# Kernel optimization log

Measured on AMD Instinct MI355X. Metric: run time of the kernel, lower is better.

The kernel has to match this reference:

```python
import jax, jax.numpy as jnp
import numpy as np

B, S, H, D = 16, 512, 12, 64          # batch, seq, heads, head_dim
HID = H * D                            # 768
MAX_POS = 512
CHAR_HP = 0.5
WORD_HP = 0.5


def setup_inputs() -> dict:
    key = jax.random.key(0)
    ks = jax.random.split(key, 12)
    s = 0.02
    return {
        "hidden_states": jax.random.normal(ks[0], (B, S, HID), jnp.float32),
        "attention_mask": jnp.zeros((B, 1, 1, S), jnp.float32),
        "character_level_matrix": jax.random.randint(ks[1], (B, S, S), 0, 8),
        "word_level_matrix": jax.random.randint(ks[2], (B, S, S), 0, 8),
        "Wq": jax.random.normal(ks[3], (HID, HID), jnp.float32) * s,
        "bq": jnp.zeros((HID,), jnp.float32),
        "Wk": jax.random.normal(ks[4], (HID, HID), jnp.float32) * s,
        "bk": jnp.zeros((HID,), jnp.float32),
        "Wv": jax.random.normal(ks[5], (HID, HID), jnp.float32) * s,
        "bv": jnp.zeros((HID,), jnp.float32),
        "dist_emb": jax.random.normal(ks[6], (2 * MAX_POS - 1, D), jnp.float32) * s,
        "char_emb": jax.random.normal(ks[7], (8, 1), jnp.float32) * s,
        "word_emb": jax.random.normal(ks[8], (8, 1), jnp.float32) * s,
    }


def reference(hidden_states, attention_mask, character_level_matrix,
              word_level_matrix, Wq, bq, Wk, bk, Wv, bv,
              dist_emb, char_emb, word_emb):
    # level nn-embedding lookup: [B,S,S] int -> [B,S,S] float
    char_bias = char_emb[character_level_matrix][..., 0]
    word_bias = word_emb[word_level_matrix][..., 0]

    def heads(x):  # [B,S,HID] -> [B,H,S,D]
        return x.reshape(B, S, H, D).transpose(0, 2, 1, 3)

    q = heads(hidden_states @ Wq.T + bq)
    k = heads(hidden_states @ Wk.T + bk)
    v = heads(hidden_states @ Wv.T + bv)

    scores = jnp.einsum('bhld,bhrd->bhlr', q, k)
    # level biases broadcast over heads
    scores = scores + CHAR_HP * char_bias[:, None] + WORD_HP * word_bias[:, None]

    # relative_key_query positional scores
    pos = jnp.arange(S)
    distance = pos[:, None] - pos[None, :]
    pe = dist_emb[distance + MAX_POS - 1]  # [S(l), S(r), D]
    scores = scores + jnp.einsum('bhld,lrd->bhlr', q, pe) \
                    + jnp.einsum('bhrd,lrd->bhlr', k, pe)

    scores = scores / jnp.sqrt(jnp.float32(D)) + attention_mask
    probs = jax.nn.softmax(scores, axis=-1)
    ctx = jnp.einsum('bhlr,bhrd->bhld', probs, v)
    return ctx.transpose(0, 2, 1, 3).reshape(B, S, HID)
```

## Files before the change

kernel.cpp:

```cpp
#include <hip/hip_runtime.h>
#include <stdint.h>

#define Bv 16
#define Sv 512
#define Hv 12
#define Dv 64
#define HIDv 768

typedef __attribute__((ext_vector_type(8))) short bf8_t;
typedef __attribute__((ext_vector_type(4))) float f32x4;
typedef __attribute__((ext_vector_type(8))) unsigned short u16x8;
typedef __attribute__((ext_vector_type(4))) unsigned short u16x4;

__device__ __forceinline__ float b2f(unsigned short u){
    union { unsigned int i; float f; } x; x.i = ((unsigned int)u) << 16; return x.f;
}
__device__ __forceinline__ unsigned short f2b(float f){
    union { float f; unsigned int i; } x; x.f = f;
    unsigned int r = x.i + 0x7fff + ((x.i >> 16) & 1);
    return (unsigned short)(r >> 16);
}
__device__ __forceinline__ void gload16(const unsigned short* g, unsigned short* l){
    __builtin_amdgcn_global_load_lds(
        (const __attribute__((address_space(1))) void*)g,
        (__attribute__((address_space(3))) void*)l, 16, 0, 0);
}

#define RS 0.18033688f
#define LOG2E 1.44269504f

__global__ void cvt_bf16(const float* __restrict__ src, unsigned short* __restrict__ dst, int n4){
    int i = blockIdx.x * 256 + threadIdx.x;
    int stride = gridDim.x * 256;
    for (; i < n4; i += stride){
        float4 v = ((const float4*)src)[i];
        u16x4 o = { f2b(v.x), f2b(v.y), f2b(v.z), f2b(v.w) };
        ((u16x4*)dst)[i] = o;
    }
}

__global__ void cvt_w3(const float* __restrict__ a, const float* __restrict__ b,
                       const float* __restrict__ c, unsigned short* __restrict__ dst, int n4each){
    int i = blockIdx.x * 256 + threadIdx.x;
    if (i >= 3*n4each) return;
    int which = i / n4each, j = i - which*n4each;
    const float* src = which == 0 ? a : (which == 1 ? b : c);
    float4 v = ((const float4*)src)[j];
    u16x4 o = { f2b(v.x), f2b(v.y), f2b(v.z), f2b(v.w) };
    ((u16x4*)dst)[i] = o;
}

__global__ __launch_bounds__(256) void prep_bias_t(
    const int* __restrict__ cmat, const int* __restrict__ wmat,
    const float* __restrict__ mask, const float* __restrict__ ce, const float* __restrict__ we,
    unsigned short* __restrict__ lvlt)
{
    __shared__ float tab[64];
    const int t = threadIdx.x;
    const int blk = blockIdx.x;
    const int c8 = blk & 7, lt = (blk >> 3) & 7, b = blk >> 6;
    if (t < 64) tab[t] = (0.5f*ce[t>>3] + 0.5f*we[t&7]) * RS;
    __syncthreads();
    const int w = t >> 6, lane = t & 63, g = lane >> 4, cc = lane & 15;
    const int ll = lt*64 + w*16 + cc;
    const int* crow = cmat + ((size_t)b*512 + ll)*512;
    const int* wrow = wmat + ((size_t)b*512 + ll)*512;
    const float* mrow = mask + (size_t)b*512;
    unsigned short o[16];
    #pragma unroll
    for (int i = 0; i < 4; ++i){
        int rb = c8*64 + i*16 + 4*g;
        int4 c4 = *(const int4*)(crow + rb);
        int4 w4 = *(const int4*)(wrow + rb);
        float4 mv = *(const float4*)(mrow + rb);
        o[i*4 + 0] = f2b(tab[(c4.x<<3)|w4.x] + mv.x * LOG2E);
        o[i*4 + 1] = f2b(tab[(c4.y<<3)|w4.y] + mv.y * LOG2E);
        o[i*4 + 2] = f2b(tab[(c4.z<<3)|w4.z] + mv.z * LOG2E);
        o[i*4 + 3] = f2b(tab[(c4.w<<3)|w4.w] + mv.w * LOG2E);
    }
    unsigned short* dst = lvlt + ((size_t)blk*256 + t)*16;
    *(u16x8*)dst       = *(u16x8*)&o[0];
    *(u16x8*)(dst + 8) = *(u16x8*)&o[8];
}

__global__ __launch_bounds__(256,3) void qkv_gemm(
    const unsigned short* __restrict__ Xb,
    const unsigned short* __restrict__ Wb,
    const float* __restrict__ bq, const float* __restrict__ bk, const float* __restrict__ bv,
    unsigned short* __restrict__ qkb,
    unsigned short* __restrict__ vtb)
{
    __shared__ unsigned short Ab[128*40];
    __shared__ unsigned short Bb[128*40];
    const int t = threadIdx.x;
    const int w = t >> 6, lane = t & 63, g = lane >> 4, cc = lane & 15;
    const int wm = w >> 1, wn = w & 1;
    const int m0 = blockIdx.x * 128;
    const int n0 = blockIdx.y * 128;

    const f32x4 fz = {0.f,0.f,0.f,0.f};
    f32x4 acc[4][4];
    #pragma unroll
    for (int i = 0; i < 4; ++i)
        #pragma unroll
        for (int j = 0; j < 4; ++j) acc[i][j] = fz;

    u16x8 pa[2], pb[2];
    #pragma unroll
    for (int r = 0; r < 2; ++r){
        int chunk = t + r*256; int row = chunk >> 2; int ch = chunk & 3;
        pa[r] = *(const u16x8*)(Xb + (size_t)(m0+row)*768 + ch*8);
        pb[r] = *(const u16x8*)(Wb + (size_t)(n0+row)*768 + ch*8);
    }
    for (int k0 = 0; k0 < 768; k0 += 32){
        __syncthreads();
        #pragma unroll
        for (int r = 0; r < 2; ++r){
            int chunk = t + r*256; int row = chunk >> 2; int ch = chunk & 3;
            *(u16x8*)&Ab[row*40 + ch*8] = pa[r];
            *(u16x8*)&Bb[row*40 + ch*8] = pb[r];
        }
        __syncthreads();
        if (k0 + 32 < 768){
            #pragma unroll
            for (int r = 0; r < 2; ++r){
                int chunk = t + r*256; int row = chunk >> 2; int ch = chunk & 3;
                pa[r] = *(const u16x8*)(Xb + (size_t)(m0+row)*768 + (k0+32) + ch*8);
                pb[r] = *(const u16x8*)(Wb + (size_t)(n0+row)*768 + (k0+32) + ch*8);
            }
        }
        bf8_t af[4], bfr[4];
        #pragma unroll
        for (int mf = 0; mf < 4; ++mf)
            af[mf] = *(const bf8_t*)&Ab[(wm*64 + mf*16 + cc)*40 + g*8];
        #pragma unroll
        for (int nf = 0; nf < 4; ++nf)
            bfr[nf] = *(const bf8_t*)&Bb[(wn*64 + nf*16 + cc)*40 + g*8];
        #pragma unroll
        for (int mf = 0; mf < 4; ++mf)
            #pragma unroll
            for (int nf = 0; nf < 4; ++nf)
                acc[mf][nf] = __builtin_amdgcn_mfma_f32_16x16x32_bf16(af[mf], bfr[nf], acc[mf][nf], 0,0,0);
    }

    const int b  = m0 >> 9;
    const int s0 = (m0 & 511) + wm*64;
    const int nbase = n0 + wn*64;
    const int proj = nbase / 768;
    const int nin0 = nbase % 768;
    const float* bias = proj == 0 ? bq : (proj == 1 ? bk : bv);
    #pragma unroll
    for (int nf = 0; nf < 4; ++nf){
        int nin = nin0 + nf*16 + cc;
        int h = nin >> 6, d = nin & 63;
        float bvv = bias[nin];
        #pragma unroll
        for (int mf = 0; mf < 4; ++mf){
            int s = s0 + mf*16 + g*4;
            if (proj < 2){
                unsigned short* base = qkb + (((((size_t)proj*Bv + b)*Hv + h)*Sv + s)*Dv + d);
                #pragma unroll
                for (int r2 = 0; r2 < 4; ++r2)
                    base[(size_t)r2*Dv] = f2b(acc[mf][nf][r2] + bvv);
            } else {
                u16x4 o = { f2b(acc[mf][nf][0]+bvv), f2b(acc[mf][nf][1]+bvv),
                            f2b(acc[mf][nf][2]+bvv), f2b(acc[mf][nf][3]+bvv) };
                *(u16x4*)(vtb + ((((size_t)b*Hv + h)*Dv + d)*Sv + s)) = o;
            }
        }
    }
}

__global__ __launch_bounds__(256,2) void attn(
    const unsigned short* __restrict__ qkb,
    const unsigned short* __restrict__ vtb,
    const unsigned short* __restrict__ deb,
    const unsigned short* __restrict__ lvlt,
    float* __restrict__ out)
{
    __shared__ __align__(16) unsigned short sm[37904];
    unsigned short* ks  = sm;
    unsigned short* vsq = sm + 4096;
    unsigned short* des = sm + 8192;
    float*          t1c = (float*)(sm + 16384);
    float*          t2c = (float*)(sm + 25360);
    unsigned int*   Pb  = (unsigned int*)(sm + 33808);

    const int t = threadIdx.x, w = t >> 6, lane = t & 63, g = lane >> 4, cc = lane & 15;
    const int lr8 = lane >> 3, lc8 = lane & 7;

    const int wg = blockIdx.x;
    const int xcd = wg & 7, inner = wg >> 3;
    const int b  = ((inner & 1) << 3) | xcd;
    const int r2 = inner >> 1;
    const int h  = r2 % 12, lt = r2 / 12;
    const int l0 = lt * 64;

    const unsigned short* qp = qkb + ((((size_t)0*Bv + b)*Hv + h)*Sv + l0)*Dv;
    const unsigned short* kp = qkb + ((((size_t)1*Bv + b)*Hv + h)*Sv)*Dv;
    const unsigned short* vp = vtb + (((size_t)b*Hv + h)*Dv)*Sv;
    const unsigned short* lvbase = lvlt + (((size_t)b*8 + lt)*8)*256*16 + (size_t)t*16;

    const f32x4 fz = {0.f,0.f,0.f,0.f};
    const int R   = 3 - w;
    const int llm = w*16 + cc;
    const int sw  = (cc & 7) << 2;
    const int d_t1 = cc - 4*g;
    const int s_t2 = 4*g + cc;

    auto stage_k = [&](int r0){
        #pragma unroll
        for (int j = 0; j < 2; ++j){
            int row = w*16 + j*8 + lr8;
            int ch  = lc8 ^ (row & 7);
            gload16(kp + (size_t)(r0 + row)*64 + ch*8, ks + w*1024 + j*512);
        }
    };
    auto stage_de = [&](int r0){
        const int base = l0 - r0 + 448;
        #pragma unroll
        for (int j = 0; j < 4; ++j){
            int row = w*32 + j*8 + lr8;
            int gr = base + row; if (gr > 1022) gr = 1022;
            int ch  = lc8 ^ (row & 7);
            gload16(deb + (size_t)gr*64 + ch*8, des + w*2048 + j*512);
        }
    };
    auto stage_v0 = [&](){
        #pragma unroll
        for (int j = 0; j < 2; ++j){
            int row = w*16 + j*8 + lr8;
            int ch  = lc8 ^ (row & 7);
            gload16(vp + (size_t)row*512 + ch*8, vsq + w*1024 + j*512);
        }
    };

    bf8_t qf0, qf1;
    {
        int qrow = w*16 + cc;
        qf0 = *(const bf8_t*)(qp + (size_t)qrow*64 + g*8);
        qf1 = *(const bf8_t*)(qp + (size_t)qrow*64 + (g+4)*8);
    }
    stage_k(0); stage_de(0); stage_v0();
    __syncthreads();

    float l_run = 0.f;
    f32x4 ctx[4] = {fz,fz,fz,fz};

    for (int c8 = 0; c8 < 8; ++c8){
        const int r0 = c8 * 64;
        u16x8 lva = *(const u16x8*)(lvbase + (size_t)c8*256*16);
        u16x8 lvb = *(const u16x8*)(lvbase + (size_t)c8*256*16 + 8);

        __builtin_amdgcn_s_setprio(1);
        f32x4 accs[4];
        bf8_t kf0, kf1;
        #pragma unroll
        for (int i = 0; i < 4; ++i){
            int row = i*16 + cc;
            bf8_t b0 = *(const bf8_t*)&ks[row*64 + ((g       ^ (row & 7))*8)];
            bf8_t b1 = *(const bf8_t*)&ks[row*64 + (((g + 4) ^ (row & 7))*8)];
            if (i == R){ kf0 = b0; kf1 = b1; }
            f32x4 a = fz;
            a = __builtin_amdgcn_mfma_f32_16x16x32_bf16(b0, qf0, a, 0,0,0);
            a = __builtin_amdgcn_mfma_f32_16x16x32_bf16(b1, qf1, a, 0,0,0);
            accs[i] = a;
        }
        #pragma unroll
        for (int i = 0; i < 5; ++i){
            int jrow = (w + i)*16 + cc;
            bf8_t d0 = *(const bf8_t*)&des[jrow*64 + ((g       ^ (jrow & 7))*8)];
            bf8_t d1 = *(const bf8_t*)&des[jrow*64 + (((g + 4) ^ (jrow & 7))*8)];
            f32x4 a1 = fz, a2 = fz;
            a1 = __builtin_amdgcn_mfma_f32_16x16x32_bf16(d0, qf0, a1, 0,0,0);
            a1 = __builtin_amdgcn_mfma_f32_16x16x32_bf16(d1, qf1, a1, 0,0,0);
            a2 = __builtin_amdgcn_mfma_f32_16x16x32_bf16(kf0, d0, a2, 0,0,0);
            a2 = __builtin_amdgcn_mfma_f32_16x16x32_bf16(kf1, d1, a2, 0,0,0);

            {
                float* tb = t1c + (cc - 16*i - 4*g + 61)*68 + llm;
                bool mA = (i != 0 || d_t1 <= 3) && (i != 4 || d_t1 >= 3);
                bool mB = (i != 0 || d_t1 <= 1) && (i != 4 || d_t1 >= 1);
                if (mA){ tb[0]   = a1[3]; tb[68]  = a1[2]; }
                if (mB){ tb[136] = a1[1]; tb[204] = a1[0]; }
            }
            {
                float* tb = t2c + (R*16 + 4*g)*66 + (16*i + 4*g + cc - 14);
                bool mA = (i != 0 || s_t2 >= 14) && (i != 4 || s_t2 <= 14);
                bool mB = (i != 0 || s_t2 >= 12) && (i != 4 || s_t2 <= 12);
                if (mA){ tb[0]   = a2[0]; tb[67]  = a2[1]; }
                if (mB){ tb[134] = a2[2]; tb[201] = a2[3]; }
            }
        }
        __builtin_amdgcn_s_setprio(0);
        __syncthreads();

        u16x8 pv0, pv1;
        if (c8 < 7){
            stage_k(r0 + 64); stage_de(r0 + 64);
            int row0 = w*16 + lr8,  ch0 = lc8 ^ (row0 & 7);
            int row1 = row0 + 8,    ch1 = lc8 ^ (row1 & 7);
            pv0 = *(const u16x8*)(vp + (size_t)row0*512 + (r0+64) + ch0*8);
            pv1 = *(const u16x8*)(vp + (size_t)row1*512 + (r0+64) + ch1*8);
        }

        float ps = 0.f;
        #pragma unroll
        for (int i = 0; i < 4; ++i){
            const float* g1 = t1c + (i*16 + 4*g + 1)*68 + llm;
            const float* g2 = t2c + (i*16 + 4*g)*66 + llm + 1;
            float t10 = g1[0], t11 = g1[68], t12 = g1[136], t13 = g1[204];
            float t20 = g2[0], t21 = g2[66], t22 = g2[132], t23 = g2[198];
            float lv0 = b2f(i < 2 ? (unsigned short)lva[i*4+0] : (unsigned short)lvb[(i-2)*4+0]);
            float lv1 = b2f(i < 2 ? (unsigned short)lva[i*4+1] : (unsigned short)lvb[(i-2)*4+1]);
            float lv2 = b2f(i < 2 ? (unsigned short)lva[i*4+2] : (unsigned short)lvb[(i-2)*4+2]);
            float lv3 = b2f(i < 2 ? (unsigned short)lva[i*4+3] : (unsigned short)lvb[(i-2)*4+3]);
            float p0 = __builtin_amdgcn_exp2f((accs[i][0] + t10 + t20) * RS + lv0);
            float p1 = __builtin_amdgcn_exp2f((accs[i][1] + t11 + t21) * RS + lv1);
            float p2 = __builtin_amdgcn_exp2f((accs[i][2] + t12 + t22) * RS + lv2);
            float p3 = __builtin_amdgcn_exp2f((accs[i][3] + t13 + t23) * RS + lv3);
            ps += (p0 + p1) + (p2 + p3);
            unsigned int prs0 = (unsigned)f2b(p0) | ((unsigned)f2b(p1) << 16);
            unsigned int prs1 = (unsigned)f2b(p2) | ((unsigned)f2b(p3) << 16);
            uint2 pr = { prs0, prs1 };
            *(uint2*)&Pb[llm*32 + ((i*8 + 2*g) ^ sw)] = pr;
        }
        ps += __shfl_xor(ps, 16);
        ps += __shfl_xor(ps, 32);
        l_run += ps;
        __builtin_amdgcn_wave_barrier();

        __builtin_amdgcn_s_setprio(1);
        #pragma unroll
        for (int kh = 0; kh < 2; ++kh){
            bf8_t pf = *(const bf8_t*)&Pb[llm*32 + ((16*kh + 4*g) ^ sw)];
            #pragma unroll
            for (int nf = 0; nf < 4; ++nf){
                int vr = nf*16 + cc;
                bf8_t vf = *(const bf8_t*)&vsq[vr*64 + (((g + 4*kh) ^ (vr & 7))*8)];
                ctx[nf] = __builtin_amdgcn_mfma_f32_16x16x32_bf16(pf, vf, ctx[nf], 0,0,0);
            }
        }
        __builtin_amdgcn_s_setprio(0);

        if (c8 < 7){
            __syncthreads();
            *(u16x8*)&vsq[w*1024 +       lane*8] = pv0;
            *(u16x8*)&vsq[w*1024 + 512 + lane*8] = pv1;
            __syncthreads();
        }
    }

    float linv[4];
    #pragma unroll
    for (int reg = 0; reg < 4; ++reg)
        linv[reg] = 1.0f / __shfl(l_run, 4*g + reg);

    #pragma unroll
    for (int nf = 0; nf < 4; ++nf){
        #pragma unroll
        for (int reg = 0; reg < 4; ++reg){
            int ll = w*16 + 4*g + reg;
            out[((size_t)b*Sv + l0 + ll)*HIDv + h*64 + nf*16 + cc] = ctx[nf][reg] * linv[reg];
        }
    }
}

extern "C" void kernel_launch(void* const* d_in, const int* in_sizes, int n_in,
                              void* d_out, int out_size, void* d_ws, size_t ws_size,
                              hipStream_t stream)
{
    const float* hs   = (const float*)d_in[0];
    const float* mask = (const float*)d_in[1];
    const int*   cmat = (const int*)  d_in[2];
    const int*   wmat = (const int*)  d_in[3];
    const float* Wq   = (const float*)d_in[4];
    const float* bq   = (const float*)d_in[5];
    const float* Wk   = (const float*)d_in[6];
    const float* bk   = (const float*)d_in[7];
    const float* Wv   = (const float*)d_in[8];
    const float* bv   = (const float*)d_in[9];
    const float* de   = (const float*)d_in[10];
    const float* ce   = (const float*)d_in[11];
    const float* we   = (const float*)d_in[12];
    float* out = (float*)d_out;

    unsigned short* Xb   = (unsigned short*)d_ws;
    unsigned short* Wb   = Xb   + 6291456;
    unsigned short* deb  = Wb   + 1769472;
    unsigned short* qkb  = deb  + 65536;
    unsigned short* vtb  = qkb  + 12582912;
    unsigned short* lvlt = vtb  + 6291456;

    cvt_bf16<<<2048, 256, 0, stream>>>(hs, Xb, 1572864);
    cvt_w3<<<1728, 256, 0, stream>>>(Wq, Wk, Wv, Wb, 147456);
    cvt_bf16<<<64,   256, 0, stream>>>(de, deb, 16368);
    prep_bias_t<<<1024, 256, 0, stream>>>(cmat, wmat, mask, ce, we, lvlt);

    qkv_gemm<<<dim3(64, 18), 256, 0, stream>>>(Xb, Wb, bq, bk, bv, qkb, vtb);
    attn<<<1536, 256, 0, stream>>>(qkb, vtb, deb, lvlt, out);
}
```

Baseline: 135.7 us.

## Merge conversion launches and co-schedule bias prep with QKV GEMM; transpose t1 cache

The three fp32-to-bf16 conversion kernels are merged into one launch, and the level-bias preparation kernel is folded into the QKV GEMM launch by interleaving prep blocks with GEMM blocks over a flat grid. This cuts launch count from six to three and lets the memory-bound bias prep overlap with the compute-bound GEMM. In the attention kernel, the relative-position t1 scratch in shared memory is transposed so each lane reads four consecutive floats with one vector load instead of four strided loads. The interleaving makes the GEMM block mapping depend on the block index, and the new scatter indices and masks for t1 must match the old ones exactly.

```diff
diff --git a/kernel.cpp b/kernel.cpp
--- a/kernel.cpp
+++ b/kernel.cpp
@@ -29,74 +29,88 @@
 #define RS 0.18033688f
 #define LOG2E 1.44269504f
 
-__global__ void cvt_bf16(const float* __restrict__ src, unsigned short* __restrict__ dst, int n4){
-    int i = blockIdx.x * 256 + threadIdx.x;
-    int stride = gridDim.x * 256;
-    for (; i < n4; i += stride){
-        float4 v = ((const float4*)src)[i];
+__global__ __launch_bounds__(256) void cvt_all(
+    const float* __restrict__ hs,
+    const float* __restrict__ Wq, const float* __restrict__ Wk, const float* __restrict__ Wv,
+    const float* __restrict__ de,
+    unsigned short* __restrict__ Xb, unsigned short* __restrict__ Wb,
+    unsigned short* __restrict__ deb)
+{
+    const int id = blockIdx.x, t = threadIdx.x;
+    if (id < 2048){
+        for (int i = id*256 + t; i < 1572864; i += 2048*256){
+            float4 v = ((const float4*)hs)[i];
+            u16x4 o = { f2b(v.x), f2b(v.y), f2b(v.z), f2b(v.w) };
+            ((u16x4*)Xb)[i] = o;
+        }
+    } else if (id < 3776){
+        int i = (id - 2048)*256 + t;
+        int which = i / 147456, j = i - which*147456;
+        const float* src = which == 0 ? Wq : (which == 1 ? Wk : Wv);
+        float4 v = ((const float4*)src)[j];
         u16x4 o = { f2b(v.x), f2b(v.y), f2b(v.z), f2b(v.w) };
-        ((u16x4*)dst)[i] = o;
-    }
-}
-
-__global__ void cvt_w3(const float* __restrict__ a, const float* __restrict__ b,
-                       const float* __restrict__ c, unsigned short* __restrict__ dst, int n4each){
-    int i = blockIdx.x * 256 + threadIdx.x;
-    if (i >= 3*n4each) return;
-    int which = i / n4each, j = i - which*n4each;
-    const float* src = which == 0 ? a : (which == 1 ? b : c);
-    float4 v = ((const float4*)src)[j];
-    u16x4 o = { f2b(v.x), f2b(v.y), f2b(v.z), f2b(v.w) };
-    ((u16x4*)dst)[i] = o;
-}
-
-__global__ __launch_bounds__(256) void prep_bias_t(
+        ((u16x4*)Wb)[i] = o;
+    } else {
+        int i = (id - 3776)*256 + t;
+        if (i < 16368){
+            float4 v = ((const float4*)de)[i];
+            u16x4 o = { f2b(v.x), f2b(v.y), f2b(v.z), f2b(v.w) };
+            ((u16x4*)deb)[i] = o;
+        }
+    }
+}
+
+__global__ __launch_bounds__(256,3) void qkv_prep(
+    const unsigned short* __restrict__ Xb,
+    const unsigned short* __restrict__ Wb,
+    const float* __restrict__ bq, const float* __restrict__ bk, const float* __restrict__ bv,
+    unsigned short* __restrict__ qkb,
+    unsigned short* __restrict__ vtb,
     const int* __restrict__ cmat, const int* __restrict__ wmat,
     const float* __restrict__ mask, const float* __restrict__ ce, const float* __restrict__ we,
     unsigned short* __restrict__ lvlt)
 {
-    __shared__ float tab[64];
-    const int t = threadIdx.x;
-    const int blk = blockIdx.x;
-    const int c8 = blk & 7, lt = (blk >> 3) & 7, b = blk >> 6;
-    if (t < 64) tab[t] = (0.5f*ce[t>>3] + 0.5f*we[t&7]) * RS;
-    __syncthreads();
-    const int w = t >> 6, lane = t & 63, g = lane >> 4, cc = lane & 15;
-    const int ll = lt*64 + w*16 + cc;
-    const int* crow = cmat + ((size_t)b*512 + ll)*512;
-    const int* wrow = wmat + ((size_t)b*512 + ll)*512;
-    const float* mrow = mask + (size_t)b*512;
-    unsigned short o[16];
-    #pragma unroll
-    for (int i = 0; i < 4; ++i){
-        int rb = c8*64 + i*16 + 4*g;
-        int4 c4 = *(const int4*)(crow + rb);
-        int4 w4 = *(const int4*)(wrow + rb);
-        float4 mv = *(const float4*)(mrow + rb);
-        o[i*4 + 0] = f2b(tab[(c4.x<<3)|w4.x] + mv.x * LOG2E);
-        o[i*4 + 1] = f2b(tab[(c4.y<<3)|w4.y] + mv.y * LOG2E);
-        o[i*4 + 2] = f2b(tab[(c4.z<<3)|w4.z] + mv.z * LOG2E);
-        o[i*4 + 3] = f2b(tab[(c4.w<<3)|w4.w] + mv.w * LOG2E);
-    }
-    unsigned short* dst = lvlt + ((size_t)blk*256 + t)*16;
-    *(u16x8*)dst       = *(u16x8*)&o[0];
-    *(u16x8*)(dst + 8) = *(u16x8*)&o[8];
-}
-
-__global__ __launch_bounds__(256,3) void qkv_gemm(
-    const unsigned short* __restrict__ Xb,
-    const unsigned short* __restrict__ Wb,
-    const float* __restrict__ bq, const float* __restrict__ bk, const float* __restrict__ bv,
-    unsigned short* __restrict__ qkb,
-    unsigned short* __restrict__ vtb)
-{
     __shared__ unsigned short Ab[128*40];
     __shared__ unsigned short Bb[128*40];
+    __shared__ float tab[64];
+
     const int t = threadIdx.x;
     const int w = t >> 6, lane = t & 63, g = lane >> 4, cc = lane & 15;
+
+    const int id = blockIdx.x;
+    const bool is_prep = (id < 2048) && (id & 1);
+
+    if (is_prep){
+        const int blk = id >> 1;
+        const int c8 = blk & 7, lt = (blk >> 3) & 7, b = blk >> 6;
+        if (t < 64) tab[t] = (0.5f*ce[t>>3] + 0.5f*we[t&7]) * RS;
+        __syncthreads();
+        const int ll = lt*64 + w*16 + cc;
+        const int* crow = cmat + ((size_t)b*512 + ll)*512;
+        const int* wrow = wmat + ((size_t)b*512 + ll)*512;
+        const float* mrow = mask + (size_t)b*512;
+        unsigned short o[16];
+        #pragma unroll
+        for (int i = 0; i < 4; ++i){
+            int rb = c8*64 + i*16 + 4*g;
+            int4 c4 = *(const int4*)(crow + rb);
+            int4 w4 = *(const int4*)(wrow + rb);
+            float4 mv = *(const float4*)(mrow + rb);
+            o[i*4 + 0] = f2b(tab[(c4.x<<3)|w4.x] + mv.x * LOG2E);
+            o[i*4 + 1] = f2b(tab[(c4.y<<3)|w4.y] + mv.y * LOG2E);
+            o[i*4 + 2] = f2b(tab[(c4.z<<3)|w4.z] + mv.z * LOG2E);
+            o[i*4 + 3] = f2b(tab[(c4.w<<3)|w4.w] + mv.w * LOG2E);
+        }
+        unsigned short* dst = lvlt + ((size_t)blk*256 + t)*16;
+        *(u16x8*)dst       = *(u16x8*)&o[0];
+        *(u16x8*)(dst + 8) = *(u16x8*)&o[8];
+        return;
+    }
+
+    const int qb = (id < 2048) ? (id >> 1) : (id - 1024);
     const int wm = w >> 1, wn = w & 1;
-    const int m0 = blockIdx.x * 128;
-    const int n0 = blockIdx.y * 128;
+    const int m0 = (qb & 63) * 128;
+    const int n0 = (qb >> 6) * 128;
 
     const f32x4 fz = {0.f,0.f,0.f,0.f};
     f32x4 acc[4][4];
@@ -178,13 +192,13 @@
     const unsigned short* __restrict__ lvlt,
     float* __restrict__ out)
 {
-    __shared__ __align__(16) unsigned short sm[37904];
+    __shared__ __align__(16) unsigned short sm[37648];
     unsigned short* ks  = sm;
     unsigned short* vsq = sm + 4096;
     unsigned short* des = sm + 8192;
-    float*          t1c = (float*)(sm + 16384);
-    float*          t2c = (float*)(sm + 25360);
-    unsigned int*   Pb  = (unsigned int*)(sm + 33808);
+    float*          t1t = (float*)(sm + 16384) + 4;
+    float*          t2c = (float*)(sm + 25104);
+    unsigned int*   Pb  = (unsigned int*)(sm + 33552);
 
     const int t = threadIdx.x, w = t >> 6, lane = t & 63, g = lane >> 4, cc = lane & 15;
     const int lr8 = lane >> 3, lc8 = lane & 7;
@@ -205,8 +219,8 @@
     const int R   = 3 - w;
     const int llm = w*16 + cc;
     const int sw  = (cc & 7) << 2;
-    const int d_t1 = cc - 4*g;
     const int s_t2 = 4*g + cc;
+    const int Kb  = cc - 4*g + 63;
 
     auto stage_k = [&](int r0){
         #pragma unroll
@@ -278,11 +292,12 @@
             a2 = __builtin_amdgcn_mfma_f32_16x16x32_bf16(kf1, d1, a2, 0,0,0);
 
             {
-                float* tb = t1c + (cc - 16*i - 4*g + 61)*68 + llm;
-                bool mA = (i != 0 || d_t1 <= 3) && (i != 4 || d_t1 >= 3);
-                bool mB = (i != 0 || d_t1 <= 1) && (i != 4 || d_t1 >= 1);
-                if (mA){ tb[0]   = a1[3]; tb[68]  = a1[2]; }
-                if (mB){ tb[136] = a1[1]; tb[204] = a1[0]; }
+                int K = Kb - 16*i;
+                float* tb = t1t + llm*68 + K;
+                bool mA = (i != 0 || K <= 64) && (i != 4 || K >= 0);
+                bool mB = (i != 0 || K <= 66) && (i != 4 || K >= 2);
+                if (mA){ tb[-1] = a1[1]; tb[0]  = a1[0]; }
+                if (mB){ tb[-3] = a1[3]; tb[-2] = a1[2]; }
             }
             {
                 float* tb = t2c + (R*16 + 4*g)*66 + (16*i + 4*g + cc - 14);
@@ -307,18 +322,17 @@
         float ps = 0.f;
         #pragma unroll
         for (int i = 0; i < 4; ++i){
-            const float* g1 = t1c + (i*16 + 4*g + 1)*68 + llm;
+            f32x4 t1v = *(const f32x4*)&t1t[llm*68 + 16*i + 4*g];
             const float* g2 = t2c + (i*16 + 4*g)*66 + llm + 1;
-            float t10 = g1[0], t11 = g1[68], t12 = g1[136], t13 = g1[204];
             float t20 = g2[0], t21 = g2[66], t22 = g2[132], t23 = g2[198];
             float lv0 = b2f(i < 2 ? (unsigned short)lva[i*4+0] : (unsigned short)lvb[(i-2)*4+0]);
             float lv1 = b2f(i < 2 ? (unsigned short)lva[i*4+1] : (unsigned short)lvb[(i-2)*4+1]);
             float lv2 = b2f(i < 2 ? (unsigned short)lva[i*4+2] : (unsigned short)lvb[(i-2)*4+2]);
             float lv3 = b2f(i < 2 ? (unsigned short)lva[i*4+3] : (unsigned short)lvb[(i-2)*4+3]);
-            float p0 = __builtin_amdgcn_exp2f((accs[i][0] + t10 + t20) * RS + lv0);
-            float p1 = __builtin_amdgcn_exp2f((accs[i][1] + t11 + t21) * RS + lv1);
-            float p2 = __builtin_amdgcn_exp2f((accs[i][2] + t12 + t22) * RS + lv2);
-            float p3 = __builtin_amdgcn_exp2f((accs[i][3] + t13 + t23) * RS + lv3);
+            float p0 = __builtin_amdgcn_exp2f((accs[i][0] + t1v[0] + t20) * RS + lv0);
+            float p1 = __builtin_amdgcn_exp2f((accs[i][1] + t1v[1] + t21) * RS + lv1);
+            float p2 = __builtin_amdgcn_exp2f((accs[i][2] + t1v[2] + t22) * RS + lv2);
+            float p3 = __builtin_amdgcn_exp2f((accs[i][3] + t1v[3] + t23) * RS + lv3);
             ps += (p0 + p1) + (p2 + p3);
             unsigned int prs0 = (unsigned)f2b(p0) | ((unsigned)f2b(p1) << 16);
             unsigned int prs1 = (unsigned)f2b(p2) | ((unsigned)f2b(p3) << 16);
@@ -392,11 +406,8 @@
     unsigned short* vtb  = qkb  + 12582912;
     unsigned short* lvlt = vtb  + 6291456;
 
-    cvt_bf16<<<2048, 256, 0, stream>>>(hs, Xb, 1572864);
-    cvt_w3<<<1728, 256, 0, stream>>>(Wq, Wk, Wv, Wb, 147456);
-    cvt_bf16<<<64,   256, 0, stream>>>(de, deb, 16368);
-    prep_bias_t<<<1024, 256, 0, stream>>>(cmat, wmat, mask, ce, we, lvlt);
-
-    qkv_gemm<<<dim3(64, 18), 256, 0, stream>>>(Xb, Wb, bq, bk, bv, qkb, vtb);
+    cvt_all<<<3840, 256, 0, stream>>>(hs, Wq, Wk, Wv, de, Xb, Wb, deb);
+    qkv_prep<<<2176, 256, 0, stream>>>(Xb, Wb, bq, bk, bv, qkb, vtb,
+                                       cmat, wmat, mask, ce, we, lvlt);
     attn<<<1536, 256, 0, stream>>>(qkb, vtb, deb, lvlt, out);
 }
```

Result: slower. 150.6 us (+10.9%).
